# Performance work log

Hardware: AMD Instinct MI355X
Metric: run time of the kernel (lower is better)

Reference implementation:

```python
import jax, jax.numpy as jnp
import numpy as np

K = 8       # branching factor == L (max child positions)
DEPTH = 6   # tree depth
NTREE = 2   # number of trees in the forest
C = 8       # hidden states
MSYM = 32   # output symbols
NGEN = 16   # parallel generative models


def _build_tree():
    starts = [(K ** d - 1) // (K - 1) for d in range(DEPTH + 2)]
    Nt = starts[DEPTH + 1]
    N = NTREE * Nt
    rng = np.random.default_rng(0)
    x = rng.integers(0, MSYM, size=N).astype(np.int32)
    local = np.arange(Nt)
    pos = np.tile(np.where(local == 0, 0, (local - 1) % K).astype(np.int32), NTREE)
    batch = np.repeat(np.arange(NTREE), Nt).astype(np.int32)
    levels = {}
    for d in range(1, DEPTH + 1):
        ch = np.concatenate([t * Nt + np.arange(starts[d], starts[d + 1]) for t in range(NTREE)]).astype(np.int32)
        upa = np.concatenate([t * Nt + np.arange(starts[d - 1], starts[d]) for t in range(NTREE)]).astype(np.int32)
        levels[d] = (ch, upa)
    return x, pos, batch, levels


def setup_inputs() -> dict:
    key = jax.random.key(0)
    kA, kB, kPi, kSP = jax.random.split(key, 4)
    x, pos, batch, levels = _build_tree()
    inp = {
        'A': jax.random.normal(kA, (C, C, K, NGEN), jnp.float32) * 2.5,
        'B': jax.random.normal(kB, (C, MSYM, NGEN), jnp.float32) * 2.5,
        'Pi': jax.random.normal(kPi, (C, K, NGEN), jnp.float32) * 2.5,
        'SP': jax.random.normal(kSP, (K, NGEN), jnp.float32) * 2.5,
        'x': jnp.asarray(x),
        'pos': jnp.asarray(pos),
        'batch': jnp.asarray(batch),
        'leaves': jnp.asarray(levels[DEPTH][0]),
    }
    for d in range(1, DEPTH + 1):
        inp[f'ch{d}'] = jnp.asarray(levels[d][0])
        inp[f'upa{d}'] = jnp.asarray(levels[d][1])
    return inp


def _upward(A, B, Pi, SP, x, pos, batch, leaves, levels):
    # softmax reparameterization (matches the per-generator per-position loops)
    smA = jax.nn.softmax(A, axis=0)    # over parent state
    smB = jax.nn.softmax(B, axis=1)    # over symbols
    smPi = jax.nn.softmax(Pi, axis=0)  # over states
    smSP = jax.nn.softmax(SP, axis=0)  # over positions

    N = x.shape[0]
    beta = jnp.zeros((N, C, NGEN), smA.dtype)
    ll = jnp.zeros((N, NGEN), smA.dtype)

    # leaves: beta = Pi[:, pos] * B[:, x], normalized per node
    b_leaf = jnp.transpose(smPi[:, pos[leaves]], (1, 0, 2)) * jnp.transpose(smB[:, x[leaves]], (1, 0, 2))  # (nl,C,G)
    nu = b_leaf.sum(1)
    beta = beta.at[leaves].set(b_leaf / nu[:, None])
    ll = ll.at[leaves].set(jnp.log(nu))

    # per-position transition weighted by position prior: (L, i_parent, j_child, G)
    Mmat = smSP[:, None, None, :] * jnp.transpose(smA, (2, 0, 1, 3))

    # upward over levels, deepest first; children of each parent are contiguous
    # with column index == child position, so scatter-add == reshape + einsum
    for ch, upa in reversed(levels):
        U = upa.shape[0]
        bch = beta[ch].reshape(U, K, C, NGEN)              # (U, pos, C_child, G)
        tb = jnp.einsum('uljg,lijg->uig', bch, Mmat)       # t_beta at parents
        bl = tb * jnp.transpose(smB[:, x[upa]], (1, 0, 2)) # (U, C, G)
        nu = bl.sum(1)
        beta = beta.at[upa].set(bl / nu[:, None])
        ll = ll.at[upa].set(jnp.log(nu))

    # sum per-node log scaling factors over each tree
    return jax.ops.segment_sum(ll, batch, num_segments=NTREE)


def reference(A, B, Pi, SP, x, pos, batch, leaves, ch1, upa1, ch2, upa2, ch3, upa3, ch4, upa4, ch5, upa5, ch6, upa6):
    levels = [(ch1, upa1), (ch2, upa2), (ch3, upa3), (ch4, upa4), (ch5, upa5), (ch6, upa6)]
    return _upward(A, B, Pi, SP, x, pos, batch, leaves, levels)
```

## Files before the change

### kernel.cpp

```cpp
#include <hip/hip_runtime.h>


constexpr int NT_NODES = 299593;
constexpr int S0 = 0, S1 = 1, S2 = 9, S3 = 73, S4 = 585, S5 = 4681, S6 = 37449;

__device__ __forceinline__ unsigned bfbits(float x) {
    unsigned v = __float_as_uint(x);
    return (v + 0x7fffu + ((v >> 16) & 1u)) >> 16;
}

__device__ __forceinline__ float sel8(const float v[8], bool c0, bool c1, bool c2) {
    float a0 = c0 ? v[1] : v[0];
    float a1 = c0 ? v[3] : v[2];
    float a2 = c0 ? v[5] : v[4];
    float a3 = c0 ? v[7] : v[6];
    float b0 = c1 ? a1 : a0;
    float b1 = c1 ? a3 : a2;
    return c2 ? b1 : b0;
}

__global__ __launch_bounds__(256) void prep(
    const float* __restrict__ A, const float* __restrict__ B,
    const float* __restrict__ Pi, const float* __restrict__ SP,
    const int* __restrict__ x,
    float* __restrict__ MtN, float* __restrict__ smBtN,
    unsigned* __restrict__ Tp, unsigned* __restrict__ EMp,
    uint4* __restrict__ rec)
{
    int bid = blockIdx.x;
    int tid = threadIdx.x;

    if (bid >= 16) {
        int pidx = (bid - 16) * 256 + tid;
        int t = pidx >> 15, localP = pidx & 32767;
        const int base = t * NT_NODES;
        const int xb = base + S6 + localP * 8;
        unsigned d0 = 0, d1 = 0;
        #pragma unroll
        for (int l = 0; l < 4; ++l) d0 |= ((unsigned)x[xb + l]) << (8 * l);
        #pragma unroll
        for (int l = 0; l < 4; ++l) d1 |= ((unsigned)x[xb + 4 + l]) << (8 * l);
        unsigned xm = (unsigned)x[base + S5 + localP];
        unsigned xr = (unsigned)x[base + S4 + (localP >> 3)];
        unsigned x3 = (unsigned)x[base + S3 + (localP >> 6)];
        rec[pidx] = make_uint4(d0, d1, xm | (xr << 8) | (x3 << 16), 0u);
        return;
    }

    int g = bid;
    __shared__ __align__(16) float mL[512];
    __shared__ __align__(16) float bLs[256];
    __shared__ __align__(16) float piLs[64];

    float sp[8];
    {
        float mx = -1e30f;
        #pragma unroll
        for (int l = 0; l < 8; ++l) { sp[l] = SP[l * 16 + g]; mx = fmaxf(mx, sp[l]); }
        float s = 0.f;
        #pragma unroll
        for (int l = 0; l < 8; ++l) { sp[l] = __expf(sp[l] - mx); s += sp[l]; }
        float r = 1.f / s;
        #pragma unroll
        for (int l = 0; l < 8; ++l) sp[l] *= r;
    }

    if (tid < 64) {
        int j = tid & 7, l = tid >> 3;
        float a[8]; float mx = -1e30f;
        #pragma unroll
        for (int i = 0; i < 8; ++i) { a[i] = A[((i * 8 + j) * 8 + l) * 16 + g]; mx = fmaxf(mx, a[i]); }
        float s = 0.f;
        #pragma unroll
        for (int i = 0; i < 8; ++i) { a[i] = __expf(a[i] - mx); s += a[i]; }
        float scale = sp[l] / s;
        #pragma unroll
        for (int i = 0; i < 8; ++i) {
            float m = a[i] * scale;
            mL[(l * 8 + j) * 8 + i] = m;
            MtN[((g * 8 + l) * 8 + j) * 8 + i] = m;
        }
    } else if (tid < 72) {
        int c = tid - 64;
        float vv[32]; float mx = -1e30f;
        #pragma unroll
        for (int m = 0; m < 32; ++m) { vv[m] = B[(c * 32 + m) * 16 + g]; mx = fmaxf(mx, vv[m]); }
        float s = 0.f;
        #pragma unroll
        for (int m = 0; m < 32; ++m) { vv[m] = __expf(vv[m] - mx); s += vv[m]; }
        float r = 1.f / s;
        #pragma unroll
        for (int m = 0; m < 32; ++m) {
            float p = vv[m] * r;
            bLs[m * 8 + c] = p;
            smBtN[(g * 32 + m) * 8 + c] = p;
        }
    } else if (tid < 80) {
        int l = tid - 72;
        float a[8]; float mx = -1e30f;
        #pragma unroll
        for (int c = 0; c < 8; ++c) { a[c] = Pi[(c * 8 + l) * 16 + g]; mx = fmaxf(mx, a[c]); }
        float s = 0.f;
        #pragma unroll
        for (int c = 0; c < 8; ++c) { a[c] = __expf(a[c] - mx); s += a[c]; }
        float r = 1.f / s;
        #pragma unroll
        for (int c = 0; c < 8; ++c) piLs[l * 8 + c] = a[c] * r;
    }
    __syncthreads();

    {
        int m = tid & 31, l = tid >> 5;
        float pb[8]; float w = 0.f;
        #pragma unroll
        for (int c = 0; c < 8; ++c) { pb[c] = piLs[l * 8 + c] * bLs[m * 8 + c]; w += pb[c]; }
        float rw = 1.f / w;
        float t[8];
        #pragma unroll
        for (int i = 0; i < 8; ++i) t[i] = 0.f;
        #pragma unroll
        for (int c = 0; c < 8; ++c) {
            float p = pb[c];
            #pragma unroll
            for (int i = 0; i < 8; ++i) t[i] = fmaf(p, mL[(l * 8 + c) * 8 + i], t[i]);
        }
        #pragma unroll
        for (int k = 0; k < 4; ++k) {
            unsigned lo = bfbits(t[2 * k] * rw), hi = bfbits(t[2 * k + 1] * rw);
            Tp[(g * 5 + k) * 256 + tid] = lo | (hi << 16);
        }
        Tp[(g * 5 + 4) * 256 + tid] = __float_as_uint(__logf(w));
    }
    if (tid < 32) {
        #pragma unroll
        for (int k = 0; k < 4; ++k) {
            unsigned lo = bfbits(bLs[tid * 8 + 2 * k]), hi = bfbits(bLs[tid * 8 + 2 * k + 1]);
            EMp[(g * 4 + k) * 32 + tid] = lo | (hi << 16);
        }
    }
}

__global__ __launch_bounds__(256, 4) void upleaf(
    const float* __restrict__ MtN, const unsigned* __restrict__ Tp,
    const unsigned* __restrict__ EMp, const uint4* __restrict__ rec,
    float* __restrict__ lv3,
    float* __restrict__ llout)
{
    __shared__ unsigned TL[256 * 5 + 32 * 5];
    __shared__ float ex[128 * 9];
    __shared__ float llp[4];

    int bid = blockIdx.x;
    int g = bid & 15;
    int pg = bid >> 4;
    int tid = threadIdx.x;
    int wave = tid >> 6;
    int lane = tid & 63;
    int half = wave & 1;
    int pairIdx = wave >> 1;
    int gu = __builtin_amdgcn_readfirstlane(g);
    int idx = pairIdx * 64 + lane;
    int s = pg * 128 + idx;
    int t = (s >= 4096) ? 1 : 0;
    int localS = s - t * 4096;

    #pragma unroll
    for (int k = 0; k < 5; ++k)
        TL[tid * 5 + k] = Tp[(gu * 5 + k) * 256 + tid];
    if (tid < 32) {
        #pragma unroll
        for (int k = 0; k < 4; ++k)
            TL[1280 + tid * 5 + k] = EMp[(gu * 4 + k) * 32 + tid];
    }

    uint4 rc[4];
    {
        const uint4* rp = rec + ((size_t)t * 32768 + (size_t)localS * 8 + half * 4);
        #pragma unroll
        for (int u = 0; u < 4; ++u) rc[u] = rp[u];
    }
    unsigned meta = rc[0].z;
    int xr = (meta >> 8) & 255;
    unsigned x3b = (meta >> 16) & 255;
    __syncthreads();

    float ll = 0.f;
    float bm[32];

    #pragma unroll
    for (int u = 0; u < 4; ++u) {
        int xl[8];
        xl[0] = rc[u].x & 255; xl[1] = (rc[u].x >> 8) & 255;
        xl[2] = (rc[u].x >> 16) & 255; xl[3] = rc[u].x >> 24;
        xl[4] = rc[u].y & 255; xl[5] = (rc[u].y >> 8) & 255;
        xl[6] = (rc[u].y >> 16) & 255; xl[7] = rc[u].y >> 24;
        int xm = rc[u].z & 255;

        float pa[8] = {0.f, 0.f, 0.f, 0.f, 0.f, 0.f, 0.f, 0.f};
        #pragma unroll
        for (int l = 0; l < 8; ++l) {
            int r5 = (l * 32 + xl[l]) * 5;
            unsigned u0 = TL[r5], u1 = TL[r5 + 1], u2 = TL[r5 + 2], u3 = TL[r5 + 3];
            ll += __uint_as_float(TL[r5 + 4]);
            pa[0] += __uint_as_float(u0 << 16); pa[1] += __uint_as_float(u0 & 0xffff0000u);
            pa[2] += __uint_as_float(u1 << 16); pa[3] += __uint_as_float(u1 & 0xffff0000u);
            pa[4] += __uint_as_float(u2 << 16); pa[5] += __uint_as_float(u2 & 0xffff0000u);
            pa[6] += __uint_as_float(u3 << 16); pa[7] += __uint_as_float(u3 & 0xffff0000u);
        }
        int e5 = 1280 + xm * 5;
        unsigned e0 = TL[e5], e1 = TL[e5 + 1], e2 = TL[e5 + 2], e3 = TL[e5 + 3];
        pa[0] *= __uint_as_float(e0 << 16); pa[1] *= __uint_as_float(e0 & 0xffff0000u);
        pa[2] *= __uint_as_float(e1 << 16); pa[3] *= __uint_as_float(e1 & 0xffff0000u);
        pa[4] *= __uint_as_float(e2 << 16); pa[5] *= __uint_as_float(e2 & 0xffff0000u);
        pa[6] *= __uint_as_float(e3 << 16); pa[7] *= __uint_as_float(e3 & 0xffff0000u);
        float nu = ((pa[0] + pa[1]) + (pa[2] + pa[3])) + ((pa[4] + pa[5]) + (pa[6] + pa[7]));
        ll += __logf(nu);
        float rn = __builtin_amdgcn_rcpf(nu);
        #pragma unroll
        for (int c = 0; c < 8; ++c) bm[u * 8 + c] = pa[c] * rn;
    }

    float pr[8] = {0.f, 0.f, 0.f, 0.f, 0.f, 0.f, 0.f, 0.f};
    {
        const float* Mg = MtN + (gu << 9) + (half << 8);
        #pragma unroll
        for (int k = 0; k < 32; ++k) {
            float b = bm[k];
            #pragma unroll
            for (int i = 0; i < 8; ++i) pr[i] = fmaf(b, Mg[k * 8 + i], pr[i]);
        }
    }
    if (half) {
        #pragma unroll
        for (int c = 0; c < 8; ++c) ex[idx * 9 + c] = pr[c];
    }
    __syncthreads();
    if (!half) {
        float tot[8];
        #pragma unroll
        for (int c = 0; c < 8; ++c) tot[c] = pr[c] + ex[idx * 9 + c];
        int e5 = 1280 + xr * 5;
        unsigned e0 = TL[e5], e1 = TL[e5 + 1], e2 = TL[e5 + 2], e3 = TL[e5 + 3];
        tot[0] *= __uint_as_float(e0 << 16); tot[1] *= __uint_as_float(e0 & 0xffff0000u);
        tot[2] *= __uint_as_float(e1 << 16); tot[3] *= __uint_as_float(e1 & 0xffff0000u);
        tot[4] *= __uint_as_float(e2 << 16); tot[5] *= __uint_as_float(e2 & 0xffff0000u);
        tot[6] *= __uint_as_float(e3 << 16); tot[7] *= __uint_as_float(e3 & 0xffff0000u);
        float nur = ((tot[0] + tot[1]) + (tot[2] + tot[3])) + ((tot[4] + tot[5]) + (tot[6] + tot[7]));
        ll += __logf(nur);
        float rr = __builtin_amdgcn_rcpf(nur);
        #pragma unroll
        for (int c = 0; c < 8; ++c) ex[idx * 9 + c] = tot[c] * rr;
        ex[idx * 9 + 8] = __uint_as_float(x3b);
    }
    __syncthreads();

    if (tid < 128) {
        int o = tid >> 3, j = tid & 7;
        int s3 = pg * 16 + o;
        float bch[8];
        #pragma unroll
        for (int l = 0; l < 8; ++l) bch[l] = ex[(o * 8 + l) * 9 + j];
        float pr3[8] = {0.f, 0.f, 0.f, 0.f, 0.f, 0.f, 0.f, 0.f};
        #pragma unroll
        for (int l = 0; l < 8; ++l) {
            const float4* mp = (const float4*)(MtN + (gu << 9) + (l << 6) + (j << 3));
            float4 m0 = mp[0], m1 = mp[1];
            float b = bch[l];
            pr3[0] = fmaf(b, m0.x, pr3[0]); pr3[1] = fmaf(b, m0.y, pr3[1]);
            pr3[2] = fmaf(b, m0.z, pr3[2]); pr3[3] = fmaf(b, m0.w, pr3[3]);
            pr3[4] = fmaf(b, m1.x, pr3[4]); pr3[5] = fmaf(b, m1.y, pr3[5]);
            pr3[6] = fmaf(b, m1.z, pr3[6]); pr3[7] = fmaf(b, m1.w, pr3[7]);
        }
        #pragma unroll
        for (int m = 1; m <= 4; m <<= 1) {
            #pragma unroll
            for (int i = 0; i < 8; ++i) pr3[i] += __shfl_xor(pr3[i], m);
        }
        int xn = (int)__float_as_uint(ex[(o * 8) * 9 + 8]);
        int e5 = 1280 + xn * 5;
        unsigned e0 = TL[e5], e1 = TL[e5 + 1], e2 = TL[e5 + 2], e3 = TL[e5 + 3];
        pr3[0] *= __uint_as_float(e0 << 16); pr3[1] *= __uint_as_float(e0 & 0xffff0000u);
        pr3[2] *= __uint_as_float(e1 << 16); pr3[3] *= __uint_as_float(e1 & 0xffff0000u);
        pr3[4] *= __uint_as_float(e2 << 16); pr3[5] *= __uint_as_float(e2 & 0xffff0000u);
        pr3[6] *= __uint_as_float(e3 << 16); pr3[7] *= __uint_as_float(e3 & 0xffff0000u);
        float nur = ((pr3[0] + pr3[1]) + (pr3[2] + pr3[3])) + ((pr3[4] + pr3[5]) + (pr3[6] + pr3[7]));
        float rr = __builtin_amdgcn_rcpf(nur);
        if (j == 0) {
            ll += __logf(nur);
            float4* dp = (float4*)(lv3 + ((size_t)g * 1024 + s3) * 8);
            dp[0] = make_float4(pr3[0] * rr, pr3[1] * rr, pr3[2] * rr, pr3[3] * rr);
            dp[1] = make_float4(pr3[4] * rr, pr3[5] * rr, pr3[6] * rr, pr3[7] * rr);
        }
    }

    #pragma unroll
    for (int m = 1; m < 64; m <<= 1) ll += __shfl_xor(ll, m);
    if (lane == 0) llp[wave] = ll;
    __syncthreads();
    if (tid == 0) llout[gu * 64 + pg] = (llp[0] + llp[1]) + (llp[2] + llp[3]);
}

__global__ __launch_bounds__(256) void uptop(
    const float* __restrict__ MtN, const float* __restrict__ smBtN,
    const int* __restrict__ x,
    const float* __restrict__ lv3,
    const float* __restrict__ ll1,
    float* __restrict__ out)
{
    int g = blockIdx.x;
    int tid = threadIdx.x;
    __shared__ __align__(16) float bet2[128 * 8];
    __shared__ __align__(16) float bet1[16 * 8];
    __shared__ float redA[256], redB[256];

    float ll0 = 0.f, llt1 = 0.f;
    if (tid < 64) {
        float v = ll1[g * 64 + tid];
        if (tid < 32) ll0 = v; else llt1 = v;
    }

    const float* Mg = MtN + (g << 9);

    if (tid < 128) {
        int t = tid >> 6, n2 = tid & 63;
        float bch[64];
        const float4* sp = (const float4*)(lv3 + ((size_t)g * 1024 + t * 512 + n2 * 8) * 8);
        #pragma unroll
        for (int v = 0; v < 16; ++v) {
            float4 f = sp[v];
            bch[4 * v + 0] = f.x; bch[4 * v + 1] = f.y;
            bch[4 * v + 2] = f.z; bch[4 * v + 3] = f.w;
        }
        float pa[8] = {0.f, 0.f, 0.f, 0.f, 0.f, 0.f, 0.f, 0.f};
        #pragma unroll
        for (int k = 0; k < 64; ++k) {
            float b = bch[k];
            #pragma unroll
            for (int i = 0; i < 8; ++i) pa[i] = fmaf(b, Mg[k * 8 + i], pa[i]);
        }
        int x2 = x[t * NT_NODES + S2 + n2];
        const float4* ep = (const float4*)(smBtN + ((g << 5) + x2) * 8);
        float4 e0 = ep[0], e1 = ep[1];
        pa[0] *= e0.x; pa[1] *= e0.y; pa[2] *= e0.z; pa[3] *= e0.w;
        pa[4] *= e1.x; pa[5] *= e1.y; pa[6] *= e1.z; pa[7] *= e1.w;
        float nu = ((pa[0] + pa[1]) + (pa[2] + pa[3])) + ((pa[4] + pa[5]) + (pa[6] + pa[7]));
        float lg = __logf(nu);
        if (t == 0) ll0 += lg; else llt1 += lg;
        float rn = __builtin_amdgcn_rcpf(nu);
        float4* dp = (float4*)(bet2 + tid * 8);
        dp[0] = make_float4(pa[0] * rn, pa[1] * rn, pa[2] * rn, pa[3] * rn);
        dp[1] = make_float4(pa[4] * rn, pa[5] * rn, pa[6] * rn, pa[7] * rn);
    }
    __syncthreads();

    if (tid < 128) {
        int o = tid >> 3, j = tid & 7;
        int t = o >> 3, n1 = o & 7;
        bool c0 = (j & 1) != 0, c1 = (j & 2) != 0, c2 = (j & 4) != 0;
        float bch[8];
        #pragma unroll
        for (int l = 0; l < 8; ++l) bch[l] = bet2[(t * 64 + n1 * 8 + l) * 8 + j];
        float pr[8] = {0.f, 0.f, 0.f, 0.f, 0.f, 0.f, 0.f, 0.f};
        #pragma unroll
        for (int l = 0; l < 8; ++l) {
            const float4* mp = (const float4*)(MtN + (g << 9) + (l << 6) + (j << 3));
            float4 m0 = mp[0], m1 = mp[1];
            float b = bch[l];
            pr[0] = fmaf(b, m0.x, pr[0]); pr[1] = fmaf(b, m0.y, pr[1]);
            pr[2] = fmaf(b, m0.z, pr[2]); pr[3] = fmaf(b, m0.w, pr[3]);
            pr[4] = fmaf(b, m1.x, pr[4]); pr[5] = fmaf(b, m1.y, pr[5]);
            pr[6] = fmaf(b, m1.z, pr[6]); pr[7] = fmaf(b, m1.w, pr[7]);
        }
        #pragma unroll
        for (int m = 1; m <= 4; m <<= 1) {
            #pragma unroll
            for (int i = 0; i < 8; ++i) pr[i] += __shfl_xor(pr[i], m);
        }
        int x1 = x[t * NT_NODES + S1 + n1];
        const float4* ep = (const float4*)(smBtN + ((g << 5) + x1) * 8);
        float4 e0 = ep[0], e1 = ep[1];
        pr[0] *= e0.x; pr[1] *= e0.y; pr[2] *= e0.z; pr[3] *= e0.w;
        pr[4] *= e1.x; pr[5] *= e1.y; pr[6] *= e1.z; pr[7] *= e1.w;
        float nu = ((pr[0] + pr[1]) + (pr[2] + pr[3])) + ((pr[4] + pr[5]) + (pr[6] + pr[7]));
        if (j == 0) { float lg = __logf(nu); if (t == 0) ll0 += lg; else llt1 += lg; }
        float rn = __builtin_amdgcn_rcpf(nu);
        bet1[o * 8 + j] = sel8(pr, c0, c1, c2) * rn;
    }
    __syncthreads();

    if (tid < 16) {
        int t = tid >> 3, j = tid & 7;
        float bch[8];
        #pragma unroll
        for (int l = 0; l < 8; ++l) bch[l] = bet1[(t * 8 + l) * 8 + j];
        float pr[8] = {0.f, 0.f, 0.f, 0.f, 0.f, 0.f, 0.f, 0.f};
        #pragma unroll
        for (int l = 0; l < 8; ++l) {
            const float4* mp = (const float4*)(MtN + (g << 9) + (l << 6) + (j << 3));
            float4 m0 = mp[0], m1 = mp[1];
            float b = bch[l];
            pr[0] = fmaf(b, m0.x, pr[0]); pr[1] = fmaf(b, m0.y, pr[1]);
            pr[2] = fmaf(b, m0.z, pr[2]); pr[3] = fmaf(b, m0.w, pr[3]);
            pr[4] = fmaf(b, m1.x, pr[4]); pr[5] = fmaf(b, m1.y, pr[5]);
            pr[6] = fmaf(b, m1.z, pr[6]); pr[7] = fmaf(b, m1.w, pr[7]);
        }
        #pragma unroll
        for (int m = 1; m <= 4; m <<= 1) {
            #pragma unroll
            for (int i = 0; i < 8; ++i) pr[i] += __shfl_xor(pr[i], m);
        }
        int x0 = x[t * NT_NODES + S0];
        const float4* ep = (const float4*)(smBtN + ((g << 5) + x0) * 8);
        float4 e0 = ep[0], e1 = ep[1];
        pr[0] *= e0.x; pr[1] *= e0.y; pr[2] *= e0.z; pr[3] *= e0.w;
        pr[4] *= e1.x; pr[5] *= e1.y; pr[6] *= e1.z; pr[7] *= e1.w;
        float nu = ((pr[0] + pr[1]) + (pr[2] + pr[3])) + ((pr[4] + pr[5]) + (pr[6] + pr[7]));
        if (j == 0) { float lg = __logf(nu); if (t == 0) ll0 += lg; else llt1 += lg; }
    }

    redA[tid] = ll0; redB[tid] = llt1;
    __syncthreads();
    for (int step = 128; step > 0; step >>= 1) {
        if (tid < step) { redA[tid] += redA[tid + step]; redB[tid] += redB[tid + step]; }
        __syncthreads();
    }
    if (tid == 0) { out[g] = redA[0]; out[16 + g] = redB[0]; }
}

extern "C" void kernel_launch(void* const* d_in, const int* in_sizes, int n_in,
                              void* d_out, int out_size, void* d_ws, size_t ws_size,
                              hipStream_t stream)
{
    const float* A  = (const float*)d_in[0];
    const float* B  = (const float*)d_in[1];
    const float* Pi = (const float*)d_in[2];
    const float* SP = (const float*)d_in[3];
    const int*   x  = (const int*)d_in[4];

    float* ws     = (float*)d_ws;
    float* MtN    = ws;
    float* smBtN  = MtN + 8192;
    unsigned* Tp  = (unsigned*)(smBtN + 4096);
    unsigned* EMp = Tp + 20480;
    uint4* rec    = (uint4*)(EMp + 2048);
    float* lv3    = (float*)(rec + 65536);
    float* ll1    = lv3 + 131072;
    float* out    = (float*)d_out;

    prep<<<272, 256, 0, stream>>>(A, B, Pi, SP, x, MtN, smBtN, Tp, EMp, rec);
    upleaf<<<1024, 256, 0, stream>>>(MtN, Tp, EMp, rec, lv3, ll1);
    uptop<<<16, 256, 0, stream>>>(MtN, smBtN, x, lv3, ll1, out);
}
```

Before: 29.81 us.

## Split uptop per tree and pad bf16 lookup table for vector LDS loads

The top-level kernel now launches one block per (generator, tree) pair instead of one per generator, and it handles level 2 with 8-lane groups and shuffle reductions instead of a single thread running a 64-term serial loop. This is meant to shorten the serial tail of the final small kernel. Separately, the packed bf16 transition and emission table in the leaf kernel is padded from 5 to 6 words per row, so each row can be read with two 8-byte LDS loads instead of four scalar loads. The padding uses a little more shared memory.

```diff
diff --git a/kernel.cpp b/kernel.cpp
--- a/kernel.cpp
+++ b/kernel.cpp
@@ -8,6 +8,8 @@
     unsigned v = __float_as_uint(x);
     return (v + 0x7fffu + ((v >> 16) & 1u)) >> 16;
 }
+__device__ __forceinline__ float bflo(unsigned u) { return __uint_as_float(u << 16); }
+__device__ __forceinline__ float bfhi(unsigned u) { return __uint_as_float(u & 0xffff0000u); }
 
 __device__ __forceinline__ float sel8(const float v[8], bool c0, bool c1, bool c2) {
     float a0 = c0 ? v[1] : v[0];
@@ -146,7 +148,7 @@
     float* __restrict__ lv3,
     float* __restrict__ llout)
 {
-    __shared__ unsigned TL[256 * 5 + 32 * 5];
+    __shared__ __align__(16) unsigned TL[256 * 6 + 32 * 6];
     __shared__ float ex[128 * 9];
     __shared__ float llp[4];
 
@@ -166,11 +168,11 @@
 
     #pragma unroll
     for (int k = 0; k < 5; ++k)
-        TL[tid * 5 + k] = Tp[(gu * 5 + k) * 256 + tid];
+        TL[tid * 6 + k] = Tp[(gu * 5 + k) * 256 + tid];
     if (tid < 32) {
         #pragma unroll
         for (int k = 0; k < 4; ++k)
-            TL[1280 + tid * 5 + k] = EMp[(gu * 4 + k) * 32 + tid];
+            TL[1536 + tid * 6 + k] = EMp[(gu * 4 + k) * 32 + tid];
     }
 
     uint4 rc[4];
@@ -199,20 +201,22 @@
         float pa[8] = {0.f, 0.f, 0.f, 0.f, 0.f, 0.f, 0.f, 0.f};
         #pragma unroll
         for (int l = 0; l < 8; ++l) {
-            int r5 = (l * 32 + xl[l]) * 5;
-            unsigned u0 = TL[r5], u1 = TL[r5 + 1], u2 = TL[r5 + 2], u3 = TL[r5 + 3];
-            ll += __uint_as_float(TL[r5 + 4]);
-            pa[0] += __uint_as_float(u0 << 16); pa[1] += __uint_as_float(u0 & 0xffff0000u);
-            pa[2] += __uint_as_float(u1 << 16); pa[3] += __uint_as_float(u1 & 0xffff0000u);
-            pa[4] += __uint_as_float(u2 << 16); pa[5] += __uint_as_float(u2 & 0xffff0000u);
-            pa[6] += __uint_as_float(u3 << 16); pa[7] += __uint_as_float(u3 & 0xffff0000u);
-        }
-        int e5 = 1280 + xm * 5;
-        unsigned e0 = TL[e5], e1 = TL[e5 + 1], e2 = TL[e5 + 2], e3 = TL[e5 + 3];
-        pa[0] *= __uint_as_float(e0 << 16); pa[1] *= __uint_as_float(e0 & 0xffff0000u);
-        pa[2] *= __uint_as_float(e1 << 16); pa[3] *= __uint_as_float(e1 & 0xffff0000u);
-        pa[4] *= __uint_as_float(e2 << 16); pa[5] *= __uint_as_float(e2 & 0xffff0000u);
-        pa[6] *= __uint_as_float(e3 << 16); pa[7] *= __uint_as_float(e3 & 0xffff0000u);
+            int r6 = (l * 32 + xl[l]) * 6;
+            uint2 ab = *(const uint2*)(TL + r6);
+            uint2 cd = *(const uint2*)(TL + r6 + 2);
+            ll += __uint_as_float(TL[r6 + 4]);
+            pa[0] += bflo(ab.x); pa[1] += bfhi(ab.x);
+            pa[2] += bflo(ab.y); pa[3] += bfhi(ab.y);
+            pa[4] += bflo(cd.x); pa[5] += bfhi(cd.x);
+            pa[6] += bflo(cd.y); pa[7] += bfhi(cd.y);
+        }
+        int e6 = 1536 + xm * 6;
+        uint2 ab = *(const uint2*)(TL + e6);
+        uint2 cd = *(const uint2*)(TL + e6 + 2);
+        pa[0] *= bflo(ab.x); pa[1] *= bfhi(ab.x);
+        pa[2] *= bflo(ab.y); pa[3] *= bfhi(ab.y);
+        pa[4] *= bflo(cd.x); pa[5] *= bfhi(cd.x);
+        pa[6] *= bflo(cd.y); pa[7] *= bfhi(cd.y);
         float nu = ((pa[0] + pa[1]) + (pa[2] + pa[3])) + ((pa[4] + pa[5]) + (pa[6] + pa[7]));
         ll += __logf(nu);
         float rn = __builtin_amdgcn_rcpf(nu);
@@ -239,12 +243,13 @@
         float tot[8];
         #pragma unroll
         for (int c = 0; c < 8; ++c) tot[c] = pr[c] + ex[idx * 9 + c];
-        int e5 = 1280 + xr * 5;
-        unsigned e0 = TL[e5], e1 = TL[e5 + 1], e2 = TL[e5 + 2], e3 = TL[e5 + 3];
-        tot[0] *= __uint_as_float(e0 << 16); tot[1] *= __uint_as_float(e0 & 0xffff0000u);
-        tot[2] *= __uint_as_float(e1 << 16); tot[3] *= __uint_as_float(e1 & 0xffff0000u);
-        tot[4] *= __uint_as_float(e2 << 16); tot[5] *= __uint_as_float(e2 & 0xffff0000u);
-        tot[6] *= __uint_as_float(e3 << 16); tot[7] *= __uint_as_float(e3 & 0xffff0000u);
+        int e6 = 1536 + xr * 6;
+        uint2 ab = *(const uint2*)(TL + e6);
+        uint2 cd = *(const uint2*)(TL + e6 + 2);
+        tot[0] *= bflo(ab.x); tot[1] *= bfhi(ab.x);
+        tot[2] *= bflo(ab.y); tot[3] *= bfhi(ab.y);
+        tot[4] *= bflo(cd.x); tot[5] *= bfhi(cd.x);
+        tot[6] *= bflo(cd.y); tot[7] *= bfhi(cd.y);
         float nur = ((tot[0] + tot[1]) + (tot[2] + tot[3])) + ((tot[4] + tot[5]) + (tot[6] + tot[7]));
         ll += __logf(nur);
         float rr = __builtin_amdgcn_rcpf(nur);
@@ -277,12 +282,13 @@
             for (int i = 0; i < 8; ++i) pr3[i] += __shfl_xor(pr3[i], m);
         }
         int xn = (int)__float_as_uint(ex[(o * 8) * 9 + 8]);
-        int e5 = 1280 + xn * 5;
-        unsigned e0 = TL[e5], e1 = TL[e5 + 1], e2 = TL[e5 + 2], e3 = TL[e5 + 3];
-        pr3[0] *= __uint_as_float(e0 << 16); pr3[1] *= __uint_as_float(e0 & 0xffff0000u);
-        pr3[2] *= __uint_as_float(e1 << 16); pr3[3] *= __uint_as_float(e1 & 0xffff0000u);
-        pr3[4] *= __uint_as_float(e2 << 16); pr3[5] *= __uint_as_float(e2 & 0xffff0000u);
-        pr3[6] *= __uint_as_float(e3 << 16); pr3[7] *= __uint_as_float(e3 & 0xffff0000u);
+        int e6 = 1536 + xn * 6;
+        uint2 ab = *(const uint2*)(TL + e6);
+        uint2 cd = *(const uint2*)(TL + e6 + 2);
+        pr3[0] *= bflo(ab.x); pr3[1] *= bfhi(ab.x);
+        pr3[2] *= bflo(ab.y); pr3[3] *= bfhi(ab.y);
+        pr3[4] *= bflo(cd.x); pr3[5] *= bfhi(cd.x);
+        pr3[6] *= bflo(cd.y); pr3[7] *= bfhi(cd.y);
         float nur = ((pr3[0] + pr3[1]) + (pr3[2] + pr3[3])) + ((pr3[4] + pr3[5]) + (pr3[6] + pr3[7]));
         float rr = __builtin_amdgcn_rcpf(nur);
         if (j == 0) {
@@ -307,59 +313,26 @@
     const float* __restrict__ ll1,
     float* __restrict__ out)
 {
-    int g = blockIdx.x;
+    int bid = blockIdx.x;
+    int g = bid & 15, t = bid >> 4;
     int tid = threadIdx.x;
-    __shared__ __align__(16) float bet2[128 * 8];
-    __shared__ __align__(16) float bet1[16 * 8];
-    __shared__ float redA[256], redB[256];
-
-    float ll0 = 0.f, llt1 = 0.f;
-    if (tid < 64) {
-        float v = ll1[g * 64 + tid];
-        if (tid < 32) ll0 = v; else llt1 = v;
-    }
-
-    const float* Mg = MtN + (g << 9);
-
-    if (tid < 128) {
-        int t = tid >> 6, n2 = tid & 63;
-        float bch[64];
-        const float4* sp = (const float4*)(lv3 + ((size_t)g * 1024 + t * 512 + n2 * 8) * 8);
-        #pragma unroll
-        for (int v = 0; v < 16; ++v) {
-            float4 f = sp[v];
-            bch[4 * v + 0] = f.x; bch[4 * v + 1] = f.y;
-            bch[4 * v + 2] = f.z; bch[4 * v + 3] = f.w;
-        }
-        float pa[8] = {0.f, 0.f, 0.f, 0.f, 0.f, 0.f, 0.f, 0.f};
-        #pragma unroll
-        for (int k = 0; k < 64; ++k) {
-            float b = bch[k];
-            #pragma unroll
-            for (int i = 0; i < 8; ++i) pa[i] = fmaf(b, Mg[k * 8 + i], pa[i]);
-        }
-        int x2 = x[t * NT_NODES + S2 + n2];
-        const float4* ep = (const float4*)(smBtN + ((g << 5) + x2) * 8);
-        float4 e0 = ep[0], e1 = ep[1];
-        pa[0] *= e0.x; pa[1] *= e0.y; pa[2] *= e0.z; pa[3] *= e0.w;
-        pa[4] *= e1.x; pa[5] *= e1.y; pa[6] *= e1.z; pa[7] *= e1.w;
-        float nu = ((pa[0] + pa[1]) + (pa[2] + pa[3])) + ((pa[4] + pa[5]) + (pa[6] + pa[7]));
-        float lg = __logf(nu);
-        if (t == 0) ll0 += lg; else llt1 += lg;
-        float rn = __builtin_amdgcn_rcpf(nu);
-        float4* dp = (float4*)(bet2 + tid * 8);
-        dp[0] = make_float4(pa[0] * rn, pa[1] * rn, pa[2] * rn, pa[3] * rn);
-        dp[1] = make_float4(pa[4] * rn, pa[5] * rn, pa[6] * rn, pa[7] * rn);
-    }
-    __syncthreads();
-
-    if (tid < 128) {
-        int o = tid >> 3, j = tid & 7;
-        int t = o >> 3, n1 = o & 7;
-        bool c0 = (j & 1) != 0, c1 = (j & 2) != 0, c2 = (j & 4) != 0;
+    __shared__ __align__(16) float bet2[64 * 8];
+    __shared__ __align__(16) float bet1[8 * 8];
+    __shared__ float red[256];
+
+    float ll = 0.f;
+    if (tid < 32) ll = ll1[g * 64 + t * 32 + tid];
+
+    int o = tid >> 3, j = tid & 7;
+    bool c0 = (j & 1) != 0, c1 = (j & 2) != 0, c2 = (j & 4) != 0;
+
+    #pragma unroll
+    for (int rep = 0; rep < 2; ++rep) {
+        int n2 = rep * 32 + o;
+        const float* sb = lv3 + ((size_t)g * 1024 + t * 512 + n2 * 8) * 8 + j;
         float bch[8];
         #pragma unroll
-        for (int l = 0; l < 8; ++l) bch[l] = bet2[(t * 64 + n1 * 8 + l) * 8 + j];
+        for (int l = 0; l < 8; ++l) bch[l] = sb[l * 8];
         float pr[8] = {0.f, 0.f, 0.f, 0.f, 0.f, 0.f, 0.f, 0.f};
         #pragma unroll
         for (int l = 0; l < 8; ++l) {
@@ -376,23 +349,23 @@
             #pragma unroll
             for (int i = 0; i < 8; ++i) pr[i] += __shfl_xor(pr[i], m);
         }
-        int x1 = x[t * NT_NODES + S1 + n1];
-        const float4* ep = (const float4*)(smBtN + ((g << 5) + x1) * 8);
+        int x2 = x[t * NT_NODES + S2 + n2];
+        const float4* ep = (const float4*)(smBtN + ((g << 5) + x2) * 8);
         float4 e0 = ep[0], e1 = ep[1];
         pr[0] *= e0.x; pr[1] *= e0.y; pr[2] *= e0.z; pr[3] *= e0.w;
         pr[4] *= e1.x; pr[5] *= e1.y; pr[6] *= e1.z; pr[7] *= e1.w;
         float nu = ((pr[0] + pr[1]) + (pr[2] + pr[3])) + ((pr[4] + pr[5]) + (pr[6] + pr[7]));
-        if (j == 0) { float lg = __logf(nu); if (t == 0) ll0 += lg; else llt1 += lg; }
+        if (j == 0) ll += __logf(nu);
         float rn = __builtin_amdgcn_rcpf(nu);
-        bet1[o * 8 + j] = sel8(pr, c0, c1, c2) * rn;
-    }
-    __syncthreads();
-
-    if (tid < 16) {
-        int t = tid >> 3, j = tid & 7;
+        bet2[n2 * 8 + j] = sel8(pr, c0, c1, c2) * rn;
+    }
+    __syncthreads();
+
+    if (tid < 64) {
+        int n1 = o;
         float bch[8];
         #pragma unroll
-        for (int l = 0; l < 8; ++l) bch[l] = bet1[(t * 8 + l) * 8 + j];
+        for (int l = 0; l < 8; ++l) bch[l] = bet2[(n1 * 8 + l) * 8 + j];
         float pr[8] = {0.f, 0.f, 0.f, 0.f, 0.f, 0.f, 0.f, 0.f};
         #pragma unroll
         for (int l = 0; l < 8; ++l) {
@@ -409,22 +382,54 @@
             #pragma unroll
             for (int i = 0; i < 8; ++i) pr[i] += __shfl_xor(pr[i], m);
         }
+        int x1 = x[t * NT_NODES + S1 + n1];
+        const float4* ep = (const float4*)(smBtN + ((g << 5) + x1) * 8);
+        float4 e0 = ep[0], e1 = ep[1];
+        pr[0] *= e0.x; pr[1] *= e0.y; pr[2] *= e0.z; pr[3] *= e0.w;
+        pr[4] *= e1.x; pr[5] *= e1.y; pr[6] *= e1.z; pr[7] *= e1.w;
+        float nu = ((pr[0] + pr[1]) + (pr[2] + pr[3])) + ((pr[4] + pr[5]) + (pr[6] + pr[7]));
+        if (j == 0) ll += __logf(nu);
+        float rn = __builtin_amdgcn_rcpf(nu);
+        bet1[n1 * 8 + j] = sel8(pr, c0, c1, c2) * rn;
+    }
+    __syncthreads();
+
+    if (tid < 8) {
+        float bch[8];
+        #pragma unroll
+        for (int l = 0; l < 8; ++l) bch[l] = bet1[l * 8 + tid];
+        float pr[8] = {0.f, 0.f, 0.f, 0.f, 0.f, 0.f, 0.f, 0.f};
+        #pragma unroll
+        for (int l = 0; l < 8; ++l) {
+            const float4* mp = (const float4*)(MtN + (g << 9) + (l << 6) + (tid << 3));
+            float4 m0 = mp[0], m1 = mp[1];
+            float b = bch[l];
+            pr[0] = fmaf(b, m0.x, pr[0]); pr[1] = fmaf(b, m0.y, pr[1]);
+            pr[2] = fmaf(b, m0.z, pr[2]); pr[3] = fmaf(b, m0.w, pr[3]);
+            pr[4] = fmaf(b, m1.x, pr[4]); pr[5] = fmaf(b, m1.y, pr[5]);
+            pr[6] = fmaf(b, m1.z, pr[6]); pr[7] = fmaf(b, m1.w, pr[7]);
+        }
+        #pragma unroll
+        for (int m = 1; m <= 4; m <<= 1) {
+            #pragma unroll
+            for (int i = 0; i < 8; ++i) pr[i] += __shfl_xor(pr[i], m);
+        }
         int x0 = x[t * NT_NODES + S0];
         const float4* ep = (const float4*)(smBtN + ((g << 5) + x0) * 8);
         float4 e0 = ep[0], e1 = ep[1];
         pr[0] *= e0.x; pr[1] *= e0.y; pr[2] *= e0.z; pr[3] *= e0.w;
         pr[4] *= e1.x; pr[5] *= e1.y; pr[6] *= e1.z; pr[7] *= e1.w;
         float nu = ((pr[0] + pr[1]) + (pr[2] + pr[3])) + ((pr[4] + pr[5]) + (pr[6] + pr[7]));
-        if (j == 0) { float lg = __logf(nu); if (t == 0) ll0 += lg; else llt1 += lg; }
-    }
-
-    redA[tid] = ll0; redB[tid] = llt1;
+        if (tid == 0) ll += __logf(nu);
+    }
+
+    red[tid] = ll;
     __syncthreads();
     for (int step = 128; step > 0; step >>= 1) {
-        if (tid < step) { redA[tid] += redA[tid + step]; redB[tid] += redB[tid + step]; }
+        if (tid < step) red[tid] += red[tid + step];
         __syncthreads();
     }
-    if (tid == 0) { out[g] = redA[0]; out[16 + g] = redB[0]; }
+    if (tid == 0) out[t * 16 + g] = red[0];
 }
 
 extern "C" void kernel_launch(void* const* d_in, const int* in_sizes, int n_in,
@@ -449,5 +454,5 @@
 
     prep<<<272, 256, 0, stream>>>(A, B, Pi, SP, x, MtN, smBtN, Tp, EMp, rec);
     upleaf<<<1024, 256, 0, stream>>>(MtN, Tp, EMp, rec, lv3, ll1);
-    uptop<<<16, 256, 0, stream>>>(MtN, smBtN, x, lv3, ll1, out);
-}
+    uptop<<<32, 256, 0, stream>>>(MtN, smBtN, x, lv3, ll1, out);
+}
```

New measurement: 32.48 us. 9.0% more time.

## Fuse top-level tree reduction into upleaf via last-block atomic counter

Applied to the files above, without the earlier changes.

Removes the separate uptop kernel launch by having the last of the 32 upleaf blocks per (generator, tree) pair, detected with a threadfence and atomic counter, run the top three levels. The top work is also split per tree, so 32 blocks handle it in parallel instead of 16. This saves a launch and the gap between kernels. In exchange it adds an atomic and a fence to every block, and the counter must be reset in prep on every call.

```diff
diff --git a/kernel.cpp b/kernel.cpp
--- a/kernel.cpp
+++ b/kernel.cpp
@@ -25,7 +25,7 @@
     const int* __restrict__ x,
     float* __restrict__ MtN, float* __restrict__ smBtN,
     unsigned* __restrict__ Tp, unsigned* __restrict__ EMp,
-    uint4* __restrict__ rec)
+    uint4* __restrict__ rec, unsigned* __restrict__ cnt)
 {
     int bid = blockIdx.x;
     int tid = threadIdx.x;
@@ -48,6 +48,7 @@
     }
 
     int g = bid;
+    if (g == 0 && tid < 32) cnt[tid] = 0;
     __shared__ __align__(16) float mL[512];
     __shared__ __align__(16) float bLs[256];
     __shared__ __align__(16) float piLs[64];
@@ -141,14 +142,18 @@
 }
 
 __global__ __launch_bounds__(256, 4) void upleaf(
-    const float* __restrict__ MtN, const unsigned* __restrict__ Tp,
-    const unsigned* __restrict__ EMp, const uint4* __restrict__ rec,
+    const float* __restrict__ MtN, const float* __restrict__ smBtN,
+    const unsigned* __restrict__ Tp, const unsigned* __restrict__ EMp,
+    const uint4* __restrict__ rec, const int* __restrict__ x,
     float* __restrict__ lv3,
-    float* __restrict__ llout)
+    float* __restrict__ llout,
+    unsigned* __restrict__ cnt,
+    float* __restrict__ out)
 {
     __shared__ unsigned TL[256 * 5 + 32 * 5];
     __shared__ float ex[128 * 9];
     __shared__ float llp[4];
+    __shared__ int lastFlag;
 
     int bid = blockIdx.x;
     int g = bid & 15;
@@ -161,8 +166,8 @@
     int gu = __builtin_amdgcn_readfirstlane(g);
     int idx = pairIdx * 64 + lane;
     int s = pg * 128 + idx;
-    int t = (s >= 4096) ? 1 : 0;
-    int localS = s - t * 4096;
+    int tBlk = (pg >= 32) ? 1 : 0;
+    int localS = s - tBlk * 4096;
 
     #pragma unroll
     for (int k = 0; k < 5; ++k)
@@ -175,7 +180,7 @@
 
     uint4 rc[4];
     {
-        const uint4* rp = rec + ((size_t)t * 32768 + (size_t)localS * 8 + half * 4);
+        const uint4* rp = rec + ((size_t)tBlk * 32768 + (size_t)localS * 8 + half * 4);
         #pragma unroll
         for (int u = 0; u < 4; ++u) rc[u] = rp[u];
     }
@@ -298,133 +303,126 @@
     if (lane == 0) llp[wave] = ll;
     __syncthreads();
     if (tid == 0) llout[gu * 64 + pg] = (llp[0] + llp[1]) + (llp[2] + llp[3]);
-}
-
-__global__ __launch_bounds__(256) void uptop(
-    const float* __restrict__ MtN, const float* __restrict__ smBtN,
-    const int* __restrict__ x,
-    const float* __restrict__ lv3,
-    const float* __restrict__ ll1,
-    float* __restrict__ out)
-{
-    int g = blockIdx.x;
-    int tid = threadIdx.x;
-    __shared__ __align__(16) float bet2[128 * 8];
-    __shared__ __align__(16) float bet1[16 * 8];
-    __shared__ float redA[256], redB[256];
-
-    float ll0 = 0.f, llt1 = 0.f;
-    if (tid < 64) {
-        float v = ll1[g * 64 + tid];
-        if (tid < 32) ll0 = v; else llt1 = v;
-    }
-
-    const float* Mg = MtN + (g << 9);
-
-    if (tid < 128) {
-        int t = tid >> 6, n2 = tid & 63;
-        float bch[64];
-        const float4* sp = (const float4*)(lv3 + ((size_t)g * 1024 + t * 512 + n2 * 8) * 8);
-        #pragma unroll
-        for (int v = 0; v < 16; ++v) {
-            float4 f = sp[v];
-            bch[4 * v + 0] = f.x; bch[4 * v + 1] = f.y;
-            bch[4 * v + 2] = f.z; bch[4 * v + 3] = f.w;
-        }
-        float pa[8] = {0.f, 0.f, 0.f, 0.f, 0.f, 0.f, 0.f, 0.f};
-        #pragma unroll
-        for (int k = 0; k < 64; ++k) {
-            float b = bch[k];
-            #pragma unroll
-            for (int i = 0; i < 8; ++i) pa[i] = fmaf(b, Mg[k * 8 + i], pa[i]);
-        }
-        int x2 = x[t * NT_NODES + S2 + n2];
-        const float4* ep = (const float4*)(smBtN + ((g << 5) + x2) * 8);
-        float4 e0 = ep[0], e1 = ep[1];
-        pa[0] *= e0.x; pa[1] *= e0.y; pa[2] *= e0.z; pa[3] *= e0.w;
-        pa[4] *= e1.x; pa[5] *= e1.y; pa[6] *= e1.z; pa[7] *= e1.w;
-        float nu = ((pa[0] + pa[1]) + (pa[2] + pa[3])) + ((pa[4] + pa[5]) + (pa[6] + pa[7]));
-        float lg = __logf(nu);
-        if (t == 0) ll0 += lg; else llt1 += lg;
-        float rn = __builtin_amdgcn_rcpf(nu);
-        float4* dp = (float4*)(bet2 + tid * 8);
-        dp[0] = make_float4(pa[0] * rn, pa[1] * rn, pa[2] * rn, pa[3] * rn);
-        dp[1] = make_float4(pa[4] * rn, pa[5] * rn, pa[6] * rn, pa[7] * rn);
-    }
-    __syncthreads();
-
-    if (tid < 128) {
-        int o = tid >> 3, j = tid & 7;
-        int t = o >> 3, n1 = o & 7;
-        bool c0 = (j & 1) != 0, c1 = (j & 2) != 0, c2 = (j & 4) != 0;
+
+    __threadfence();
+    if (tid == 0) lastFlag = (atomicAdd(&cnt[gu * 2 + tBlk], 1u) == 31u);
+    __syncthreads();
+    if (!lastFlag) return;
+
+    float* bet2 = ex;
+    float* bet1 = ex + 512;
+    float* red  = ex + 576;
+
+    float llf = 0.f;
+    if (tid < 32) llf = llout[gu * 64 + tBlk * 32 + tid];
+
+    int o = tid >> 3, j = tid & 7;
+    bool c0 = (j & 1) != 0, c1 = (j & 2) != 0, c2 = (j & 4) != 0;
+
+    #pragma unroll
+    for (int rep = 0; rep < 2; ++rep) {
+        int n2 = rep * 32 + o;
+        const float* sb = lv3 + ((size_t)gu * 1024 + tBlk * 512 + n2 * 8) * 8 + j;
         float bch[8];
         #pragma unroll
-        for (int l = 0; l < 8; ++l) bch[l] = bet2[(t * 64 + n1 * 8 + l) * 8 + j];
-        float pr[8] = {0.f, 0.f, 0.f, 0.f, 0.f, 0.f, 0.f, 0.f};
+        for (int l = 0; l < 8; ++l) bch[l] = sb[l * 8];
+        float pA[8] = {0.f, 0.f, 0.f, 0.f, 0.f, 0.f, 0.f, 0.f};
         #pragma unroll
         for (int l = 0; l < 8; ++l) {
-            const float4* mp = (const float4*)(MtN + (g << 9) + (l << 6) + (j << 3));
+            const float4* mp = (const float4*)(MtN + (gu << 9) + (l << 6) + (j << 3));
             float4 m0 = mp[0], m1 = mp[1];
             float b = bch[l];
-            pr[0] = fmaf(b, m0.x, pr[0]); pr[1] = fmaf(b, m0.y, pr[1]);
-            pr[2] = fmaf(b, m0.z, pr[2]); pr[3] = fmaf(b, m0.w, pr[3]);
-            pr[4] = fmaf(b, m1.x, pr[4]); pr[5] = fmaf(b, m1.y, pr[5]);
-            pr[6] = fmaf(b, m1.z, pr[6]); pr[7] = fmaf(b, m1.w, pr[7]);
+            pA[0] = fmaf(b, m0.x, pA[0]); pA[1] = fmaf(b, m0.y, pA[1]);
+            pA[2] = fmaf(b, m0.z, pA[2]); pA[3] = fmaf(b, m0.w, pA[3]);
+            pA[4] = fmaf(b, m1.x, pA[4]); pA[5] = fmaf(b, m1.y, pA[5]);
+            pA[6] = fmaf(b, m1.z, pA[6]); pA[7] = fmaf(b, m1.w, pA[7]);
         }
         #pragma unroll
         for (int m = 1; m <= 4; m <<= 1) {
             #pragma unroll
-            for (int i = 0; i < 8; ++i) pr[i] += __shfl_xor(pr[i], m);
-        }
-        int x1 = x[t * NT_NODES + S1 + n1];
-        const float4* ep = (const float4*)(smBtN + ((g << 5) + x1) * 8);
+            for (int i = 0; i < 8; ++i) pA[i] += __shfl_xor(pA[i], m);
+        }
+        int x2 = x[tBlk * NT_NODES + S2 + n2];
+        const float4* ep = (const float4*)(smBtN + ((gu << 5) + x2) * 8);
         float4 e0 = ep[0], e1 = ep[1];
-        pr[0] *= e0.x; pr[1] *= e0.y; pr[2] *= e0.z; pr[3] *= e0.w;
-        pr[4] *= e1.x; pr[5] *= e1.y; pr[6] *= e1.z; pr[7] *= e1.w;
-        float nu = ((pr[0] + pr[1]) + (pr[2] + pr[3])) + ((pr[4] + pr[5]) + (pr[6] + pr[7]));
-        if (j == 0) { float lg = __logf(nu); if (t == 0) ll0 += lg; else llt1 += lg; }
+        pA[0] *= e0.x; pA[1] *= e0.y; pA[2] *= e0.z; pA[3] *= e0.w;
+        pA[4] *= e1.x; pA[5] *= e1.y; pA[6] *= e1.z; pA[7] *= e1.w;
+        float nu = ((pA[0] + pA[1]) + (pA[2] + pA[3])) + ((pA[4] + pA[5]) + (pA[6] + pA[7]));
+        if (j == 0) llf += __logf(nu);
         float rn = __builtin_amdgcn_rcpf(nu);
-        bet1[o * 8 + j] = sel8(pr, c0, c1, c2) * rn;
-    }
-    __syncthreads();
-
-    if (tid < 16) {
-        int t = tid >> 3, j = tid & 7;
+        bet2[n2 * 8 + j] = sel8(pA, c0, c1, c2) * rn;
+    }
+    __syncthreads();
+
+    if (tid < 64) {
+        int n1 = o;
         float bch[8];
         #pragma unroll
-        for (int l = 0; l < 8; ++l) bch[l] = bet1[(t * 8 + l) * 8 + j];
-        float pr[8] = {0.f, 0.f, 0.f, 0.f, 0.f, 0.f, 0.f, 0.f};
+        for (int l = 0; l < 8; ++l) bch[l] = bet2[(n1 * 8 + l) * 8 + j];
+        float pB[8] = {0.f, 0.f, 0.f, 0.f, 0.f, 0.f, 0.f, 0.f};
         #pragma unroll
         for (int l = 0; l < 8; ++l) {
-            const float4* mp = (const float4*)(MtN + (g << 9) + (l << 6) + (j << 3));
+            const float4* mp = (const float4*)(MtN + (gu << 9) + (l << 6) + (j << 3));
             float4 m0 = mp[0], m1 = mp[1];
             float b = bch[l];
-            pr[0] = fmaf(b, m0.x, pr[0]); pr[1] = fmaf(b, m0.y, pr[1]);
-            pr[2] = fmaf(b, m0.z, pr[2]); pr[3] = fmaf(b, m0.w, pr[3]);
-            pr[4] = fmaf(b, m1.x, pr[4]); pr[5] = fmaf(b, m1.y, pr[5]);
-            pr[6] = fmaf(b, m1.z, pr[6]); pr[7] = fmaf(b, m1.w, pr[7]);
+            pB[0] = fmaf(b, m0.x, pB[0]); pB[1] = fmaf(b, m0.y, pB[1]);
+            pB[2] = fmaf(b, m0.z, pB[2]); pB[3] = fmaf(b, m0.w, pB[3]);
+            pB[4] = fmaf(b, m1.x, pB[4]); pB[5] = fmaf(b, m1.y, pB[5]);
+            pB[6] = fmaf(b, m1.z, pB[6]); pB[7] = fmaf(b, m1.w, pB[7]);
         }
         #pragma unroll
         for (int m = 1; m <= 4; m <<= 1) {
             #pragma unroll
-            for (int i = 0; i < 8; ++i) pr[i] += __shfl_xor(pr[i], m);
-        }
-        int x0 = x[t * NT_NODES + S0];
-        const float4* ep = (const float4*)(smBtN + ((g << 5) + x0) * 8);
+            for (int i = 0; i < 8; ++i) pB[i] += __shfl_xor(pB[i], m);
+        }
+        int x1 = x[tBlk * NT_NODES + S1 + n1];
+        const float4* ep = (const float4*)(smBtN + ((gu << 5) + x1) * 8);
         float4 e0 = ep[0], e1 = ep[1];
-        pr[0] *= e0.x; pr[1] *= e0.y; pr[2] *= e0.z; pr[3] *= e0.w;
-        pr[4] *= e1.x; pr[5] *= e1.y; pr[6] *= e1.z; pr[7] *= e1.w;
-        float nu = ((pr[0] + pr[1]) + (pr[2] + pr[3])) + ((pr[4] + pr[5]) + (pr[6] + pr[7]));
-        if (j == 0) { float lg = __logf(nu); if (t == 0) ll0 += lg; else llt1 += lg; }
-    }
-
-    redA[tid] = ll0; redB[tid] = llt1;
+        pB[0] *= e0.x; pB[1] *= e0.y; pB[2] *= e0.z; pB[3] *= e0.w;
+        pB[4] *= e1.x; pB[5] *= e1.y; pB[6] *= e1.z; pB[7] *= e1.w;
+        float nu = ((pB[0] + pB[1]) + (pB[2] + pB[3])) + ((pB[4] + pB[5]) + (pB[6] + pB[7]));
+        if (j == 0) llf += __logf(nu);
+        float rn = __builtin_amdgcn_rcpf(nu);
+        bet1[n1 * 8 + j] = sel8(pB, c0, c1, c2) * rn;
+    }
+    __syncthreads();
+
+    if (tid < 8) {
+        float bch[8];
+        #pragma unroll
+        for (int l = 0; l < 8; ++l) bch[l] = bet1[l * 8 + tid];
+        float pC[8] = {0.f, 0.f, 0.f, 0.f, 0.f, 0.f, 0.f, 0.f};
+        #pragma unroll
+        for (int l = 0; l < 8; ++l) {
+            const float4* mp = (const float4*)(MtN + (gu << 9) + (l << 6) + (tid << 3));
+            float4 m0 = mp[0], m1 = mp[1];
+            float b = bch[l];
+            pC[0] = fmaf(b, m0.x, pC[0]); pC[1] = fmaf(b, m0.y, pC[1]);
+            pC[2] = fmaf(b, m0.z, pC[2]); pC[3] = fmaf(b, m0.w, pC[3]);
+            pC[4] = fmaf(b, m1.x, pC[4]); pC[5] = fmaf(b, m1.y, pC[5]);
+            pC[6] = fmaf(b, m1.z, pC[6]); pC[7] = fmaf(b, m1.w, pC[7]);
+        }
+        #pragma unroll
+        for (int m = 1; m <= 4; m <<= 1) {
+            #pragma unroll
+            for (int i = 0; i < 8; ++i) pC[i] += __shfl_xor(pC[i], m);
+        }
+        int x0 = x[tBlk * NT_NODES + S0];
+        const float4* ep = (const float4*)(smBtN + ((gu << 5) + x0) * 8);
+        float4 e0 = ep[0], e1 = ep[1];
+        pC[0] *= e0.x; pC[1] *= e0.y; pC[2] *= e0.z; pC[3] *= e0.w;
+        pC[4] *= e1.x; pC[5] *= e1.y; pC[6] *= e1.z; pC[7] *= e1.w;
+        float nu = ((pC[0] + pC[1]) + (pC[2] + pC[3])) + ((pC[4] + pC[5]) + (pC[6] + pC[7]));
+        if (tid == 0) llf += __logf(nu);
+    }
+
+    red[tid] = llf;
     __syncthreads();
     for (int step = 128; step > 0; step >>= 1) {
-        if (tid < step) { redA[tid] += redA[tid + step]; redB[tid] += redB[tid + step]; }
+        if (tid < step) red[tid] += red[tid + step];
         __syncthreads();
     }
-    if (tid == 0) { out[g] = redA[0]; out[16 + g] = redB[0]; }
+    if (tid == 0) out[tBlk * 16 + gu] = red[0];
 }
 
 extern "C" void kernel_launch(void* const* d_in, const int* in_sizes, int n_in,
@@ -445,9 +443,9 @@
     uint4* rec    = (uint4*)(EMp + 2048);
     float* lv3    = (float*)(rec + 65536);
     float* ll1    = lv3 + 131072;
+    unsigned* cnt = (unsigned*)(ll1 + 1024);
     float* out    = (float*)d_out;
 
-    prep<<<272, 256, 0, stream>>>(A, B, Pi, SP, x, MtN, smBtN, Tp, EMp, rec);
-    upleaf<<<1024, 256, 0, stream>>>(MtN, Tp, EMp, rec, lv3, ll1);
-    uptop<<<16, 256, 0, stream>>>(MtN, smBtN, x, lv3, ll1, out);
+    prep<<<272, 256, 0, stream>>>(A, B, Pi, SP, x, MtN, smBtN, Tp, EMp, rec, cnt);
+    upleaf<<<1024, 256, 0, stream>>>(MtN, smBtN, Tp, EMp, rec, x, lv3, ll1, cnt, out);
 }
```

New measurement: 108.2 us. +263.1%, slower.

## Replace per-leaf log-likelihood lookups with a symbol-position histogram dot product

Applied to the files above, without the earlier changes.

Leaf log scaling terms depend only on (position, symbol), so the prep kernel now builds a per-tree histogram of (position, symbol) counts using shared-memory atomics, then global atomics. uptop multiplies these counts by the tabulated leaf log terms, and upleaf no longer accumulates one TL lookup per leaf. This removes a shared-memory load and add per leaf from the hot kernel. In exchange it adds a memset launch, atomics in prep, and a count-times-value sum whose float rounding differs from the original order.

```diff
diff --git a/kernel.cpp b/kernel.cpp
--- a/kernel.cpp
+++ b/kernel.cpp
@@ -25,25 +25,37 @@
     const int* __restrict__ x,
     float* __restrict__ MtN, float* __restrict__ smBtN,
     unsigned* __restrict__ Tp, unsigned* __restrict__ EMp,
-    uint4* __restrict__ rec)
+    uint4* __restrict__ rec, int* __restrict__ cntLM)
 {
     int bid = blockIdx.x;
     int tid = threadIdx.x;
 
     if (bid >= 16) {
+        __shared__ int h[256];
+        h[tid] = 0;
+        __syncthreads();
+
         int pidx = (bid - 16) * 256 + tid;
         int t = pidx >> 15, localP = pidx & 32767;
         const int base = t * NT_NODES;
         const int xb = base + S6 + localP * 8;
+        int xs[8];
+        #pragma unroll
+        for (int l = 0; l < 8; ++l) xs[l] = x[xb + l];
         unsigned d0 = 0, d1 = 0;
         #pragma unroll
-        for (int l = 0; l < 4; ++l) d0 |= ((unsigned)x[xb + l]) << (8 * l);
-        #pragma unroll
-        for (int l = 0; l < 4; ++l) d1 |= ((unsigned)x[xb + 4 + l]) << (8 * l);
+        for (int l = 0; l < 4; ++l) d0 |= ((unsigned)xs[l]) << (8 * l);
+        #pragma unroll
+        for (int l = 0; l < 4; ++l) d1 |= ((unsigned)xs[4 + l]) << (8 * l);
         unsigned xm = (unsigned)x[base + S5 + localP];
         unsigned xr = (unsigned)x[base + S4 + (localP >> 3)];
         unsigned x3 = (unsigned)x[base + S3 + (localP >> 6)];
         rec[pidx] = make_uint4(d0, d1, xm | (xr << 8) | (x3 << 16), 0u);
+
+        #pragma unroll
+        for (int l = 0; l < 8; ++l) atomicAdd(&h[l * 32 + xs[l]], 1);
+        __syncthreads();
+        if (h[tid]) atomicAdd(&cntLM[t * 256 + tid], h[tid]);
         return;
     }
 
@@ -201,7 +213,6 @@
         for (int l = 0; l < 8; ++l) {
             int r5 = (l * 32 + xl[l]) * 5;
             unsigned u0 = TL[r5], u1 = TL[r5 + 1], u2 = TL[r5 + 2], u3 = TL[r5 + 3];
-            ll += __uint_as_float(TL[r5 + 4]);
             pa[0] += __uint_as_float(u0 << 16); pa[1] += __uint_as_float(u0 & 0xffff0000u);
             pa[2] += __uint_as_float(u1 << 16); pa[3] += __uint_as_float(u1 & 0xffff0000u);
             pa[4] += __uint_as_float(u2 << 16); pa[5] += __uint_as_float(u2 & 0xffff0000u);
@@ -305,6 +316,8 @@
     const int* __restrict__ x,
     const float* __restrict__ lv3,
     const float* __restrict__ ll1,
+    const unsigned* __restrict__ Tp,
+    const int* __restrict__ cntLM,
     float* __restrict__ out)
 {
     int g = blockIdx.x;
@@ -317,6 +330,11 @@
     if (tid < 64) {
         float v = ll1[g * 64 + tid];
         if (tid < 32) ll0 = v; else llt1 = v;
+    }
+    {
+        float lt = __uint_as_float(Tp[(g * 5 + 4) * 256 + tid]);
+        ll0  += (float)cntLM[tid]       * lt;
+        llt1 += (float)cntLM[256 + tid] * lt;
     }
 
     const float* Mg = MtN + (g << 9);
@@ -445,9 +463,11 @@
     uint4* rec    = (uint4*)(EMp + 2048);
     float* lv3    = (float*)(rec + 65536);
     float* ll1    = lv3 + 131072;
+    int* cntLM    = (int*)(ll1 + 1024);
     float* out    = (float*)d_out;
 
-    prep<<<272, 256, 0, stream>>>(A, B, Pi, SP, x, MtN, smBtN, Tp, EMp, rec);
+    hipMemsetAsync(cntLM, 0, 512 * sizeof(int), stream);
+    prep<<<272, 256, 0, stream>>>(A, B, Pi, SP, x, MtN, smBtN, Tp, EMp, rec, cntLM);
     upleaf<<<1024, 256, 0, stream>>>(MtN, Tp, EMp, rec, lv3, ll1);
-    uptop<<<16, 256, 0, stream>>>(MtN, smBtN, x, lv3, ll1, out);
-}
+    uptop<<<16, 256, 0, stream>>>(MtN, smBtN, x, lv3, ll1, Tp, cntLM, out);
+}
```

New measurement: 35.02 us. +17.5%, slower.
